# Performance work log

Measured on AMD Instinct MI355X. Metric: run time of the kernel, lower is better.

## Reference

```python
import jax, jax.numpy as jnp
import numpy as np

DIM = 1024
MLP_MULT = 4
NUM_EXPERTS = 8
EXPERT_HIDDEN = MLP_MULT * DIM // NUM_EXPERTS  # 512


def setup_inputs() -> dict:
    key = jax.random.key(0)
    k_x, k_r, k_fc, k_pj = jax.random.split(key, 4)
    x = jax.random.normal(k_x, (4, 4096, DIM), dtype=jnp.float32)
    # router: nn.Linear(dim, num_experts, bias=False) -> weight [E, D]
    w_router = jax.random.normal(k_r, (NUM_EXPERTS, DIM), dtype=jnp.float32) * (1.0 / np.sqrt(DIM))
    # per-expert fc: Linear(dim, hidden) weight [H, D]; stacked [E, H, D]
    w_fc = jax.random.normal(k_fc, (NUM_EXPERTS, EXPERT_HIDDEN, DIM), dtype=jnp.float32) * (1.0 / np.sqrt(DIM))
    # per-expert proj: Linear(hidden, dim) weight [D, H]; stacked [E, D, H]
    # (_zero_init in the original; use small random values so the reference output is non-trivial)
    w_proj = jax.random.normal(k_pj, (NUM_EXPERTS, DIM, EXPERT_HIDDEN), dtype=jnp.float32) * (1.0 / np.sqrt(EXPERT_HIDDEN))
    return {"x": x, "w_router": w_router, "w_fc": w_fc, "w_proj": w_proj}


def reference(x, w_router, w_fc, w_proj):
    # Router on detached input; top-1 expert per token.
    logits = jnp.einsum('bsd,ed->bse', jax.lax.stop_gradient(x), w_router)
    weights = jax.nn.softmax(logits, axis=-1)  # computed as in original (unused in output)
    indices = jnp.argmax(weights, axis=-1)     # [B, S]
    onehot = jax.nn.one_hot(indices, NUM_EXPERTS, dtype=x.dtype)  # [B, S, E]
    # Dense dispatch: run all experts, combine with one-hot (equivalent to mask gather/scatter).
    h = jnp.einsum('bsd,ehd->bseh', x, w_fc)              # [B, S, E, H]
    h = jnp.where(h >= 0, h, 0.5 * h)                      # leaky_relu(negative_slope=0.5)
    h = h * h                                              # square
    out = jnp.einsum('bseh,edh,bse->bsd', h, w_proj, onehot)
    return out
```

## Files before the change

### kernel.cpp

```cpp
#include <hip/hip_runtime.h>
#include <stdint.h>
#include <stddef.h>

#define DIM 1024
#define NEXP 8
#define HID 512
#define NTOK 16384
#define NB_HIST 64

typedef __attribute__((ext_vector_type(4))) float f32x4;
typedef __attribute__((ext_vector_type(8))) short short8;
typedef __attribute__((ext_vector_type(4))) unsigned short u16x4;

__device__ __forceinline__ unsigned short f2b(float f) {
  unsigned int u = __float_as_uint(f);
  return (unsigned short)((u + 0x7FFFu + ((u >> 16) & 1u)) >> 16);
}

__device__ __forceinline__ void gload_lds16(const unsigned short* g, unsigned short* l) {
  __builtin_amdgcn_global_load_lds((const __attribute__((address_space(1))) void*)g,
                                   (__attribute__((address_space(3))) void*)l, 16, 0, 0);
}

__global__ __launch_bounds__(256) void k_router(const float* __restrict__ x,
                                                const float* __restrict__ wr,
                                                int* __restrict__ eid,
                                                unsigned short* __restrict__ xb) {
  int wid = threadIdx.x >> 6, lane = threadIdx.x & 63;
  int tok = blockIdx.x * 4 + wid;
  const float* xr = x + (size_t)tok * DIM;
  unsigned short* xbr = xb + (size_t)tok * DIM;
  float s[NEXP];
#pragma unroll
  for (int e = 0; e < NEXP; e++) s[e] = 0.f;
#pragma unroll
  for (int i = 0; i < 4; i++) {
    f32x4 xv = *(const f32x4*)(xr + lane * 4 + 256 * i);
    u16x4 u;
    u.x = f2b(xv.x); u.y = f2b(xv.y); u.z = f2b(xv.z); u.w = f2b(xv.w);
    *(u16x4*)(xbr + lane * 4 + 256 * i) = u;
#pragma unroll
    for (int e = 0; e < NEXP; e++) {
      f32x4 wv = *(const f32x4*)(wr + e * DIM + lane * 4 + 256 * i);
      s[e] += xv.x * wv.x + xv.y * wv.y + xv.z * wv.z + xv.w * wv.w;
    }
  }
#pragma unroll
  for (int e = 0; e < NEXP; e++) {
    float v = s[e];
#pragma unroll
    for (int off = 32; off > 0; off >>= 1) v += __shfl_xor(v, off);
    s[e] = v;
  }
  if (lane == 0) {
    int be = 0;
    float bv = s[0];
#pragma unroll
    for (int e = 1; e < NEXP; e++) {
      if (s[e] > bv) { bv = s[e]; be = e; }
    }
    eid[tok] = be;
  }
}

__global__ __launch_bounds__(256) void k_hist(const int* __restrict__ eid,
                                              int* __restrict__ bc) {
  __shared__ int h[NEXP];
  if (threadIdx.x < NEXP) h[threadIdx.x] = 0;
  __syncthreads();
  int tok = blockIdx.x * (NTOK / NB_HIST) + threadIdx.x;
  atomicAdd(&h[eid[tok]], 1);
  __syncthreads();
  if (threadIdx.x < NEXP) bc[blockIdx.x * NEXP + threadIdx.x] = h[threadIdx.x];
}

__global__ void k_scan(const int* __restrict__ bc, int* __restrict__ offs,
                       int* __restrict__ base) {
  __shared__ int cnt[NEXP];
  __shared__ int so[NEXP + 1];
  int t = threadIdx.x;
  if (t < NEXP) {
    int run = 0;
    for (int b = 0; b < NB_HIST; b++) {
      base[b * NEXP + t] = run;
      run += bc[b * NEXP + t];
    }
    cnt[t] = run;
  }
  __syncthreads();
  if (t == 0) {
    int a = 0;
    for (int e = 0; e < NEXP; e++) { so[e] = a; a += cnt[e]; }
    so[NEXP] = a;
  }
  __syncthreads();
  if (t < NEXP + 1) offs[t] = so[t];
  for (int i = t; i < NB_HIST * NEXP; i += blockDim.x) base[i] += so[i % NEXP];
}

__global__ __launch_bounds__(256) void k_scatter(const int* __restrict__ eid,
                                                 const int* __restrict__ base,
                                                 int* __restrict__ tlist) {
  __shared__ int cur[NEXP];
  if (threadIdx.x < NEXP) cur[threadIdx.x] = base[blockIdx.x * NEXP + threadIdx.x];
  __syncthreads();
  int tok = blockIdx.x * (NTOK / NB_HIST) + threadIdx.x;
  int e = eid[tok];
  int pos = atomicAdd(&cur[e], 1);
  tlist[pos] = tok;
}

__global__ __launch_bounds__(256) void k_cast(const float* __restrict__ a,
                                              const float* __restrict__ b,
                                              unsigned short* __restrict__ oa,
                                              unsigned short* __restrict__ ob) {
  const int n4 = NEXP * HID * DIM / 4;
  int stride = gridDim.x * blockDim.x;
  for (int i = blockIdx.x * blockDim.x + threadIdx.x; i < n4; i += stride) {
    f32x4 va = ((const f32x4*)a)[i];
    f32x4 vb = ((const f32x4*)b)[i];
    u16x4 ua, ub;
    ua.x = f2b(va.x); ua.y = f2b(va.y); ua.z = f2b(va.z); ua.w = f2b(va.w);
    ub.x = f2b(vb.x); ub.y = f2b(vb.y); ub.z = f2b(vb.z); ub.w = f2b(vb.w);
    ((u16x4*)oa)[i] = ua;
    ((u16x4*)ob)[i] = ub;
  }
}

template <int KDIM, int NDIM, int NB, bool IS_FC>
__global__ __launch_bounds__(256) void k_gemm(
    const unsigned short* __restrict__ xb, const unsigned short* __restrict__ hin,
    const unsigned short* __restrict__ wb, const int* __restrict__ offs,
    const int* __restrict__ tlist, unsigned short* __restrict__ hout,
    float* __restrict__ out) {
  int l = ((int)blockIdx.x & 7) * ((int)gridDim.x >> 3) + ((int)blockIdx.x >> 3);
  int e = -1, mb = 0, nb = 0, acc2 = 0;
#pragma unroll
  for (int i = 0; i < NEXP; i++) {
    int mi = offs[i + 1] - offs[i];
    int tb = ((mi + 127) >> 7) * NB;
    if (e < 0 && l < acc2 + tb) {
      int r = l - acc2;
      e = i; mb = r / NB; nb = r % NB;
    }
    acc2 += tb;
  }
  if (e < 0) return;
  int off = offs[e];
  int me = offs[e + 1] - off;
  int m0 = mb * 128;
  int n0 = nb * 128;

  __shared__ unsigned short lds[3][2][128 * 32];

  int t = threadIdx.x;
  int lane = t & 63, w = t >> 6;
  int wm = w >> 1, wn = w & 1;

  int kb = (lane & 3) ^ ((lane >> 2) & 3);

  const unsigned short* asrc[2];
  const unsigned short* bsrc[2];
#pragma unroll
  for (int i = 0; i < 2; i++) {
    int r = i * 64 + w * 16 + (lane >> 2);
    int gm = m0 + r;
    if (gm > me - 1) gm = me - 1;
    if (IS_FC) {
      int tok = tlist[off + gm];
      asrc[i] = xb + (size_t)tok * KDIM + kb * 8;
    } else {
      asrc[i] = hin + (size_t)(off + gm) * KDIM + kb * 8;
    }
    bsrc[i] = wb + ((size_t)e * NDIM + n0 + r) * (size_t)KDIM + kb * 8;
  }

  f32x4 acc[4][4] = {};
  const int NT = KDIM / 32;

  unsigned short* b0a = &lds[0][0][0]; unsigned short* b0b = &lds[0][1][0];
  unsigned short* b1a = &lds[1][0][0]; unsigned short* b1b = &lds[1][1][0];
  unsigned short* b2a = &lds[2][0][0]; unsigned short* b2b = &lds[2][1][0];

#define STAGE(kt_, da_, db_)                                   \
  do {                                                         \
    gload_lds16(asrc[0] + (kt_) * 32, (da_) + (w * 16) * 32);  \
    gload_lds16(asrc[1] + (kt_) * 32, (da_) + (64 + w * 16) * 32); \
    gload_lds16(bsrc[0] + (kt_) * 32, (db_) + (w * 16) * 32);  \
    gload_lds16(bsrc[1] + (kt_) * 32, (db_) + (64 + w * 16) * 32); \
  } while (0)

  STAGE(0, b0a, b0b);
  STAGE(1, b1a, b1b);

  for (int kt = 0; kt < NT; kt++) {
    if (kt < NT - 1) {
      asm volatile("s_waitcnt vmcnt(4)" ::: "memory");
    } else {
      asm volatile("s_waitcnt vmcnt(0)" ::: "memory");
    }
    __builtin_amdgcn_s_barrier();

    if (kt + 2 < NT) STAGE(kt + 2, b2a, b2b);

    short8 af[4], bf[4];
#pragma unroll
    for (int i = 0; i < 4; i++) {
      int ra = wm * 64 + i * 16 + (lane & 15);
      int ca = (lane >> 4) ^ (ra & 3);
      af[i] = *(const short8*)&b0a[ra * 32 + ca * 8];
      int rb = wn * 64 + i * 16 + (lane & 15);
      int cb = (lane >> 4) ^ (rb & 3);
      bf[i] = *(const short8*)&b0b[rb * 32 + cb * 8];
    }
    __builtin_amdgcn_s_setprio(1);
#pragma unroll
    for (int mi = 0; mi < 4; mi++)
#pragma unroll
      for (int ni = 0; ni < 4; ni++)
        acc[mi][ni] =
            __builtin_amdgcn_mfma_f32_16x16x32_bf16(af[mi], bf[ni], acc[mi][ni], 0, 0, 0);
    __builtin_amdgcn_s_setprio(0);

    unsigned short* ta = b0a; b0a = b1a; b1a = b2a; b2a = ta;
    unsigned short* tb = b0b; b0b = b1b; b1b = b2b; b2b = tb;
  }
#undef STAGE

  int rb = (lane >> 4) * 4, cb = lane & 15;
#pragma unroll
  for (int mi = 0; mi < 4; mi++) {
#pragma unroll
    for (int j = 0; j < 4; j++) {
      int ml = wm * 64 + mi * 16 + rb + j;
      if (m0 + ml < me) {
        if (IS_FC) {
#pragma unroll
          for (int ni = 0; ni < 4; ni++) {
            int col = n0 + wn * 64 + ni * 16 + cb;
            float v = acc[mi][ni][j];
            v = (v >= 0.f) ? v * v : 0.25f * v * v;
            hout[(size_t)(off + m0 + ml) * HID + col] = f2b(v);
          }
        } else {
          int tok = tlist[off + m0 + ml];
#pragma unroll
          for (int ni = 0; ni < 4; ni++) {
            int col = n0 + wn * 64 + ni * 16 + cb;
            out[(size_t)tok * DIM + col] = acc[mi][ni][j];
          }
        }
      }
    }
  }
}

extern "C" void kernel_launch(void* const* d_in, const int* in_sizes, int n_in,
                              void* d_out, int out_size, void* d_ws, size_t ws_size,
                              hipStream_t stream) {
  const float* x = (const float*)d_in[0];
  const float* wr = (const float*)d_in[1];
  const float* wfc = (const float*)d_in[2];
  const float* wpj = (const float*)d_in[3];
  float* out = (float*)d_out;

  uintptr_t p = (uintptr_t)d_ws;
  int* offs = (int*)p;  p += 256;
  int* bc = (int*)p;    p += sizeof(int) * NB_HIST * NEXP;
  int* base = (int*)p;  p += sizeof(int) * NB_HIST * NEXP;
  int* eid = (int*)p;   p += sizeof(int) * NTOK;
  int* tlist = (int*)p; p += sizeof(int) * NTOK;
  unsigned short* wfc_b = (unsigned short*)p; p += (size_t)NEXP * HID * DIM * 2;
  unsigned short* wpj_b = (unsigned short*)p; p += (size_t)NEXP * DIM * HID * 2;
  unsigned short* hbuf = (unsigned short*)p;  p += (size_t)NTOK * HID * 2;
  unsigned short* xb = (unsigned short*)p;    p += (size_t)NTOK * DIM * 2;

  k_router<<<NTOK / 4, 256, 0, stream>>>(x, wr, eid, xb);
  k_cast<<<1024, 256, 0, stream>>>(wfc, wpj, wfc_b, wpj_b);
  k_hist<<<NB_HIST, 256, 0, stream>>>(eid, bc);
  k_scan<<<1, 256, 0, stream>>>(bc, offs, base);
  k_scatter<<<NB_HIST, 256, 0, stream>>>(eid, base, tlist);
  k_gemm<1024, 512, 4, true><<<dim3(544), 256, 0, stream>>>(
      xb, nullptr, wfc_b, offs, tlist, hbuf, nullptr);
  k_gemm<512, 1024, 8, false><<<dim3(1080), 256, 0, stream>>>(
      nullptr, hbuf, wpj_b, offs, tlist, nullptr, out);
}
```

Before: 112.6 us.

## Fuse router and weight cast into one launch, four tokens per wave

Merges the router kernel and the weight bf16 cast kernel into a single launch, with disjoint block ranges running each role concurrently. Each router wave now handles four tokens, so every router weight load is reused across four tokens and far fewer blocks are launched. This removes one kernel launch and the gap between the two memory-bound passes. The cost is higher register use per thread and a cast pass that now runs on only 512 blocks.

```diff
diff --git a/kernel.cpp b/kernel.cpp
--- a/kernel.cpp
+++ b/kernel.cpp
@@ -7,6 +7,8 @@
 #define HID 512
 #define NTOK 16384
 #define NB_HIST 64
+#define NB_ROUTER 1024
+#define NB_CAST 512
 
 typedef __attribute__((ext_vector_type(4))) float f32x4;
 typedef __attribute__((ext_vector_type(8))) short short8;
@@ -22,44 +24,73 @@
                                    (__attribute__((address_space(3))) void*)l, 16, 0, 0);
 }
 
-__global__ __launch_bounds__(256) void k_router(const float* __restrict__ x,
-                                                const float* __restrict__ wr,
-                                                int* __restrict__ eid,
-                                                unsigned short* __restrict__ xb) {
-  int wid = threadIdx.x >> 6, lane = threadIdx.x & 63;
-  int tok = blockIdx.x * 4 + wid;
-  const float* xr = x + (size_t)tok * DIM;
-  unsigned short* xbr = xb + (size_t)tok * DIM;
-  float s[NEXP];
-#pragma unroll
-  for (int e = 0; e < NEXP; e++) s[e] = 0.f;
-#pragma unroll
-  for (int i = 0; i < 4; i++) {
-    f32x4 xv = *(const f32x4*)(xr + lane * 4 + 256 * i);
-    u16x4 u;
-    u.x = f2b(xv.x); u.y = f2b(xv.y); u.z = f2b(xv.z); u.w = f2b(xv.w);
-    *(u16x4*)(xbr + lane * 4 + 256 * i) = u;
-#pragma unroll
-    for (int e = 0; e < NEXP; e++) {
-      f32x4 wv = *(const f32x4*)(wr + e * DIM + lane * 4 + 256 * i);
-      s[e] += xv.x * wv.x + xv.y * wv.y + xv.z * wv.z + xv.w * wv.w;
-    }
-  }
-#pragma unroll
-  for (int e = 0; e < NEXP; e++) {
-    float v = s[e];
-#pragma unroll
-    for (int off = 32; off > 0; off >>= 1) v += __shfl_xor(v, off);
-    s[e] = v;
-  }
-  if (lane == 0) {
-    int be = 0;
-    float bv = s[0];
-#pragma unroll
-    for (int e = 1; e < NEXP; e++) {
-      if (s[e] > bv) { bv = s[e]; be = e; }
-    }
-    eid[tok] = be;
+__global__ __launch_bounds__(256) void k_router_cast(
+    const float* __restrict__ x, const float* __restrict__ wr,
+    int* __restrict__ eid, unsigned short* __restrict__ xb,
+    const float* __restrict__ wfc, const float* __restrict__ wpj,
+    unsigned short* __restrict__ oa, unsigned short* __restrict__ ob) {
+  int bid = blockIdx.x;
+  if (bid < NB_ROUTER) {
+    int w = threadIdx.x >> 6, lane = threadIdx.x & 63;
+    int t0 = bid * 16 + w * 4;
+    const float* xr = x + (size_t)t0 * DIM;
+    unsigned short* xbr = xb + (size_t)t0 * DIM;
+    float s[4][NEXP];
+#pragma unroll
+    for (int j = 0; j < 4; j++)
+#pragma unroll
+      for (int e = 0; e < NEXP; e++) s[j][e] = 0.f;
+#pragma unroll
+    for (int i = 0; i < 4; i++) {
+      f32x4 xv[4];
+#pragma unroll
+      for (int j = 0; j < 4; j++) {
+        xv[j] = *(const f32x4*)(xr + j * DIM + lane * 4 + 256 * i);
+        u16x4 u;
+        u.x = f2b(xv[j].x); u.y = f2b(xv[j].y); u.z = f2b(xv[j].z); u.w = f2b(xv[j].w);
+        *(u16x4*)(xbr + j * DIM + lane * 4 + 256 * i) = u;
+      }
+#pragma unroll
+      for (int e = 0; e < NEXP; e++) {
+        f32x4 wv = *(const f32x4*)(wr + e * DIM + lane * 4 + 256 * i);
+#pragma unroll
+        for (int j = 0; j < 4; j++)
+          s[j][e] += xv[j].x * wv.x + xv[j].y * wv.y + xv[j].z * wv.z + xv[j].w * wv.w;
+      }
+    }
+#pragma unroll
+    for (int j = 0; j < 4; j++)
+#pragma unroll
+      for (int e = 0; e < NEXP; e++) {
+        float v = s[j][e];
+#pragma unroll
+        for (int off = 32; off > 0; off >>= 1) v += __shfl_xor(v, off);
+        s[j][e] = v;
+      }
+    if (lane == 0) {
+#pragma unroll
+      for (int j = 0; j < 4; j++) {
+        int be = 0;
+        float bv = s[j][0];
+#pragma unroll
+        for (int e = 1; e < NEXP; e++) {
+          if (s[j][e] > bv) { bv = s[j][e]; be = e; }
+        }
+        eid[t0 + j] = be;
+      }
+    }
+  } else {
+    const int n4 = NEXP * HID * DIM / 4;
+    int stride = NB_CAST * 256;
+    for (int i = (bid - NB_ROUTER) * 256 + (int)threadIdx.x; i < n4; i += stride) {
+      f32x4 va = ((const f32x4*)wfc)[i];
+      f32x4 vb = ((const f32x4*)wpj)[i];
+      u16x4 ua, ub;
+      ua.x = f2b(va.x); ua.y = f2b(va.y); ua.z = f2b(va.z); ua.w = f2b(va.w);
+      ub.x = f2b(vb.x); ub.y = f2b(vb.y); ub.z = f2b(vb.z); ub.w = f2b(vb.w);
+      ((u16x4*)oa)[i] = ua;
+      ((u16x4*)ob)[i] = ub;
+    }
   }
 }
 
@@ -110,23 +141,6 @@
   tlist[pos] = tok;
 }
 
-__global__ __launch_bounds__(256) void k_cast(const float* __restrict__ a,
-                                              const float* __restrict__ b,
-                                              unsigned short* __restrict__ oa,
-                                              unsigned short* __restrict__ ob) {
-  const int n4 = NEXP * HID * DIM / 4;
-  int stride = gridDim.x * blockDim.x;
-  for (int i = blockIdx.x * blockDim.x + threadIdx.x; i < n4; i += stride) {
-    f32x4 va = ((const f32x4*)a)[i];
-    f32x4 vb = ((const f32x4*)b)[i];
-    u16x4 ua, ub;
-    ua.x = f2b(va.x); ua.y = f2b(va.y); ua.z = f2b(va.z); ua.w = f2b(va.w);
-    ub.x = f2b(vb.x); ub.y = f2b(vb.y); ub.z = f2b(vb.z); ub.w = f2b(vb.w);
-    ((u16x4*)oa)[i] = ua;
-    ((u16x4*)ob)[i] = ub;
-  }
-}
-
 template <int KDIM, int NDIM, int NB, bool IS_FC>
 __global__ __launch_bounds__(256) void k_gemm(
     const unsigned short* __restrict__ xb, const unsigned short* __restrict__ hin,
@@ -275,8 +289,8 @@
   unsigned short* hbuf = (unsigned short*)p;  p += (size_t)NTOK * HID * 2;
   unsigned short* xb = (unsigned short*)p;    p += (size_t)NTOK * DIM * 2;
 
-  k_router<<<NTOK / 4, 256, 0, stream>>>(x, wr, eid, xb);
-  k_cast<<<1024, 256, 0, stream>>>(wfc, wpj, wfc_b, wpj_b);
+  k_router_cast<<<NB_ROUTER + NB_CAST, 256, 0, stream>>>(
+      x, wr, eid, xb, wfc, wpj, wfc_b, wpj_b);
   k_hist<<<NB_HIST, 256, 0, stream>>>(eid, bc);
   k_scan<<<1, 256, 0, stream>>>(bc, offs, base);
   k_scatter<<<NB_HIST, 256, 0, stream>>>(eid, base, tlist);
```

Result: no change. 111.3 us (-1.2%).
